# Optimization experiments

Measured on AMD Instinct MI355X. Metric: run time of the kernel, lower is better.

The kernel has to match this reference:

```python
import jax, jax.numpy as jnp
import numpy as np
import math

NUM_HEADS = 16
EMBED_DIM = 1024
DIM_HEAD = EMBED_DIM // NUM_HEADS


def setup_inputs() -> dict:
    key = jax.random.key(0)
    k_x, k_wi, k_bi, k_wo, k_bo = jax.random.split(key, 5)
    B, S, D = 2, 2048, EMBED_DIM
    scale = 1.0 / math.sqrt(D)
    return {
        "x": jax.random.normal(k_x, (B, S, D), dtype=jnp.float32),
        "w_in": jax.random.normal(k_wi, (3 * D, D), dtype=jnp.float32) * scale,
        "b_in": jax.random.normal(k_bi, (3 * D,), dtype=jnp.float32) * 0.02,
        "w_out": jax.random.normal(k_wo, (D, D), dtype=jnp.float32) * scale,
        "b_out": jax.random.normal(k_bo, (D,), dtype=jnp.float32) * 0.02,
    }


def reference(x, w_in, b_in, w_out, b_out):
    B, S, D = x.shape
    H, Dh = NUM_HEADS, DIM_HEAD
    # in_proj: x @ w_in.T + b_in -> chunk into q, k, v
    qkv = jnp.einsum("bsd,ed->bse", x, w_in) + b_in  # [B,S,3D]
    q, k, v = jnp.split(qkv, 3, axis=-1)
    q = q.reshape(B, S, H, Dh).transpose(0, 2, 1, 3)  # [B,H,S,Dh]
    k = k.reshape(B, S, H, Dh).transpose(0, 2, 1, 3)
    v = v.reshape(B, S, H, Dh).transpose(0, 2, 1, 3)
    # scores, causal mask (masked_fill before scaling == after, since -inf/c = -inf)
    scores = jnp.einsum("bhqd,bhkd->bhqk", q, k) / math.sqrt(Dh)
    causal = jnp.triu(jnp.ones((S, S), dtype=bool), k=1)
    scores = jnp.where(causal, -jnp.inf, scores)
    weight = jax.nn.softmax(scores, axis=-1)
    out = jnp.einsum("bhqk,bhkd->bhqd", weight, v)  # [B,H,S,Dh]
    out = out.transpose(0, 2, 1, 3).reshape(B, S, D)
    return jnp.einsum("bsd,ed->bse", out, w_out) + b_out
```

## Files before the change

kernel.cpp:

```cpp
#include <hip/hip_runtime.h>
#include <stdint.h>

typedef unsigned short u16;
typedef float f32x4 __attribute__((ext_vector_type(4)));
typedef __bf16 bf16x8 __attribute__((ext_vector_type(8)));

#define AS1 __attribute__((address_space(1)))
#define AS3 __attribute__((address_space(3)))

#define QK_SCALE 0.18033688011112042f

__device__ __forceinline__ u16 f32_to_bf16(float f) {
    unsigned u = __float_as_uint(f);
    unsigned r = u + 0x7fffu + ((u >> 16) & 1u);
    return (u16)(r >> 16);
}

__device__ __forceinline__ float bf16_f(u16 u) {
    return __uint_as_float(((unsigned)u) << 16);
}

__device__ __forceinline__ void gload_lds16(const u16* g, u16* l) {
    __builtin_amdgcn_global_load_lds((const AS1 unsigned int*)g,
                                     (AS3 unsigned int*)l, 16, 0, 0);
}

__device__ __forceinline__ int swz(int row, int col8) {
    return row * 64 + (((col8 ^ (row & 7)) & 7) << 3);
}
__device__ __forceinline__ int swzv(int row, int col8) {
    return row * 64 + (((col8 ^ row ^ (row >> 3)) & 7) << 3);
}

__global__ __launch_bounds__(256) void cvt_bf16_3(const float4* __restrict__ in0,
                                                  const float4* __restrict__ in1,
                                                  const float4* __restrict__ in2,
                                                  uint2* __restrict__ out,
                                                  int n0, int n1, int ntot) {
    for (int i = blockIdx.x * blockDim.x + threadIdx.x; i < ntot;
         i += gridDim.x * blockDim.x) {
        float4 v;
        if (i < n0) v = in0[i];
        else if (i < n0 + n1) {
            v = in1[i - n0];
            if (((i - n0) >> 8) < 1024) {
                v.x *= QK_SCALE; v.y *= QK_SCALE; v.z *= QK_SCALE; v.w *= QK_SCALE;
            }
        } else v = in2[i - n0 - n1];
        uint2 o;
        o.x = (unsigned)f32_to_bf16(v.x) | ((unsigned)f32_to_bf16(v.y) << 16);
        o.y = (unsigned)f32_to_bf16(v.z) | ((unsigned)f32_to_bf16(v.w) << 16);
        out[i] = o;
    }
}

template <int BNT, bool BF16_OUT>
__global__ __launch_bounds__(512, 2) void gemm_ring(const u16* __restrict__ A,
                                                    const u16* __restrict__ B,
                                                    const float* __restrict__ bias,
                                                    void* __restrict__ Cv,
                                                    int M, int N, int K,
                                                    int qcols, float qscale) {
    extern __shared__ u16 lds[];
    constexpr int NACC = BNT / 64;
    constexpr int NCH = (128 + BNT) >> 7;
    constexpr int ASZ = 128 * 32;
    constexpr int BSZ = BNT * 32;
    const int t = threadIdx.x;
    const int l = t & 63, w = t >> 6;
    const int lr = l & 15, lhi = l >> 4;
    const int wm = w >> 2, wn = w & 3;
    const int orig = blockIdx.y * gridDim.x + blockIdx.x;
    const int sid = (orig & 7) * 32 + (orig >> 3);
    const int bm = sid & 31, bn = sid >> 5;

    const u16* Ag = A + (size_t)bm * 128 * K;
    const u16* Bg = B + (size_t)bn * BNT * K;

    auto STAGE = [&](int kt, int slot) {
        u16* As = lds + slot * ASZ;
        u16* Bs = lds + 4 * ASZ + slot * BSZ;
        {
            int c = t, row = c >> 2, cp = c & 3;
            int gc = (cp ^ ((row >> 1) & 3)) << 3;
            gload_lds16(Ag + (size_t)row * K + kt * 32 + gc, As + c * 8);
        }
        #pragma unroll
        for (int i = 0; i < NCH - 1; ++i) {
            int c = i * 512 + t, row = c >> 2, cp = c & 3;
            int gc = (cp ^ ((row >> 1) & 3)) << 3;
            gload_lds16(Bg + (size_t)row * K + kt * 32 + gc, Bs + c * 8);
        }
    };

    f32x4 acc[4][NACC] = {};
    const int NT = K >> 5;
    STAGE(0, 0);
    STAGE(1, 1);
    STAGE(2, 2);

    const int ckey = (lr >> 1) & 3;

    for (int kt = 0; kt < NT; ++kt) {
        if (kt < NT - 2) {
            if constexpr (NCH == 4) asm volatile("s_waitcnt vmcnt(8)" ::: "memory");
            else                    asm volatile("s_waitcnt vmcnt(4)" ::: "memory");
        } else if (kt == NT - 2) {
            if constexpr (NCH == 4) asm volatile("s_waitcnt vmcnt(4)" ::: "memory");
            else                    asm volatile("s_waitcnt vmcnt(2)" ::: "memory");
        } else {
            asm volatile("s_waitcnt vmcnt(0)" ::: "memory");
        }
        __builtin_amdgcn_s_barrier();
        __builtin_amdgcn_sched_barrier(0);

        if (kt + 3 < NT) STAGE(kt + 3, (kt + 3) & 3);

        const u16* As = lds + (kt & 3) * ASZ;
        const u16* Bs = lds + 4 * ASZ + (kt & 3) * BSZ;
        bf16x8 af[4], bfv[NACC];
        #pragma unroll
        for (int m = 0; m < 4; ++m) {
            int row = wm * 64 + m * 16 + lr;
            af[m] = *(const bf16x8*)(As + row * 32 + ((lhi ^ ckey) << 3));
        }
        #pragma unroll
        for (int n = 0; n < NACC; ++n) {
            int row = wn * (BNT / 4) + n * 16 + lr;
            bfv[n] = *(const bf16x8*)(Bs + row * 32 + ((lhi ^ ckey) << 3));
        }
        __builtin_amdgcn_s_setprio(1);
        #pragma unroll
        for (int m = 0; m < 4; ++m)
            #pragma unroll
            for (int n = 0; n < NACC; ++n)
                acc[m][n] = __builtin_amdgcn_mfma_f32_16x16x32_bf16(
                    af[m], bfv[n], acc[m][n], 0, 0, 0);
        __builtin_amdgcn_s_setprio(0);
    }

    const int row0 = bm * 128 + wm * 64 + lhi * 4;
    const int col0 = bn * BNT + wn * (BNT / 4) + lr;
    #pragma unroll
    for (int n = 0; n < NACC; ++n) {
        int col = col0 + n * 16;
        float bv = bias[col];
        if (col < qcols) bv *= qscale;
        #pragma unroll
        for (int m = 0; m < 4; ++m)
            #pragma unroll
            for (int r = 0; r < 4; ++r) {
                int row = row0 + m * 16 + r;
                float v = acc[m][n][r] + bv;
                if constexpr (BF16_OUT)
                    ((u16*)Cv)[(size_t)row * N + col] = f32_to_bf16(v);
                else
                    ((float*)Cv)[(size_t)row * N + col] = v;
            }
    }
}

__device__ __forceinline__ void write_vt(u16* vt, uint4 a, uint4 b, int g, int cl) {
    unsigned aw[4] = {a.x, a.y, a.z, a.w};
    unsigned bw[4] = {b.x, b.y, b.z, b.w};
    #pragma unroll
    for (int j = 0; j < 8; ++j) {
        int dh = cl * 8 + j;
        unsigned sel = (j & 1) ? 0x07060302u : 0x05040100u;
        unsigned v = __builtin_amdgcn_perm(bw[j >> 1], aw[j >> 1], sel);
        *(unsigned*)(vt + swzv(dh, g >> 2) + (2 * g & 7)) = v;
    }
}

__global__ __launch_bounds__(512, 4) void attn_kernel(const u16* __restrict__ qkv,
                                                      u16* __restrict__ out) {
    __shared__ u16 Ks[2][2][64 * 64];
    __shared__ u16 Vt[2][64 * 64];
    __shared__ u16 Ps[8][16 * 64];
    const int t = threadIdx.x;
    const int w = t >> 6, l = t & 63;
    const int lr = l & 15, lhi = l >> 4;
    const int par = w >> 2, wl = w & 3;
    const int tp = t & 255;
    const int orig = blockIdx.x;
    const int sid = (orig & 7) * 64 + (orig >> 3);
    const int bh = sid >> 4, bi = sid & 15;
    const int h = bh & 15, b = bh >> 4;

    const u16* Kg = qkv + ((size_t)(b * 2048)) * 3072 + 1024 + h * 64;
    const u16* Vg = qkv + ((size_t)(b * 2048)) * 3072 + 2048 + h * 64;
    const int vg = tp >> 3, vcl = tp & 7;
    u16* Pw = Ps[w];
    unsigned* Pst = (unsigned*)Pw;
    float2* mlX = (float2*)&Ks[0][0][0];

    #pragma unroll 1
    for (int pass = 0; pass < 2; ++pass) {
        const int qt = pass ? (31 - bi) : bi;
        __syncthreads();

        const u16* Qrow = qkv + ((size_t)(b * 2048 + qt * 64 + wl * 16 + lr)) * 3072 + h * 64;
        bf16x8 qf0 = *(const bf16x8*)(Qrow + lhi * 8);
        bf16x8 qf1 = *(const bf16x8*)(Qrow + 32 + lhi * 8);

        uint4 va = {0, 0, 0, 0}, vbr = {0, 0, 0, 0};
        if (par <= qt) {
            #pragma unroll
            for (int i = 0; i < 2; ++i) {
                int c = i * 256 + tp, r = c >> 3, cl = c & 7;
                gload_lds16(Kg + ((size_t)(par * 64 + r)) * 3072 + ((cl ^ (r & 7)) << 3),
                            &Ks[par][0][c * 8]);
            }
            va = *(const uint4*)(Vg + ((size_t)(par * 64 + 2 * vg)) * 3072 + vcl * 8);
            vbr = *(const uint4*)(Vg + ((size_t)(par * 64 + 2 * vg + 1)) * 3072 + vcl * 8);
            write_vt(Vt[par], va, vbr, vg, vcl);
        }
        __syncthreads();

        f32x4 acc[4] = {};
        float m_run = -1e30f, l_run = 0.f;
        int cur = 0;
        const int nt = (qt >> 1) + 1;

        for (int it = 0; it < nt; ++it) {
            const int t64 = 2 * it + par;
            const bool active = (t64 <= qt);
            const bool pfv = (t64 + 2 <= qt);
            if (pfv) {
                #pragma unroll
                for (int i = 0; i < 2; ++i) {
                    int c = i * 256 + tp, r = c >> 3, cl = c & 7;
                    gload_lds16(Kg + ((size_t)((t64 + 2) * 64 + r)) * 3072 +
                                    ((cl ^ (r & 7)) << 3),
                                &Ks[par][cur ^ 1][c * 8]);
                }
                va = *(const uint4*)(Vg + ((size_t)((t64 + 2) * 64 + 2 * vg)) * 3072 + vcl * 8);
                vbr = *(const uint4*)(Vg + ((size_t)((t64 + 2) * 64 + 2 * vg + 1)) * 3072 + vcl * 8);
            }

            if (active) {
                f32x4 sv[4] = {};
                __builtin_amdgcn_s_setprio(1);
                #pragma unroll
                for (int kks = 0; kks < 2; ++kks) {
                    #pragma unroll
                    for (int n = 0; n < 4; ++n) {
                        bf16x8 kf = *(const bf16x8*)(&Ks[par][cur][swz(n * 16 + lr, kks * 4 + lhi)]);
                        sv[n] = __builtin_amdgcn_mfma_f32_16x16x32_bf16(
                            kf, kks ? qf1 : qf0, sv[n], 0, 0, 0);
                    }
                }
                __builtin_amdgcn_s_setprio(0);

                if (t64 == qt) {
                    #pragma unroll
                    for (int n = 0; n < 4; ++n)
                        #pragma unroll
                        for (int r = 0; r < 4; ++r)
                            if ((n * 16 + lhi * 4 + r) > (wl * 16 + lr)) sv[n][r] = -1e30f;
                }
                float t0 = fmaxf(fmaxf(sv[0][0], sv[0][1]), fmaxf(sv[0][2], sv[0][3]));
                float t1 = fmaxf(fmaxf(sv[1][0], sv[1][1]), fmaxf(sv[1][2], sv[1][3]));
                float t2 = fmaxf(fmaxf(sv[2][0], sv[2][1]), fmaxf(sv[2][2], sv[2][3]));
                float t3 = fmaxf(fmaxf(sv[3][0], sv[3][1]), fmaxf(sv[3][2], sv[3][3]));
                float mx = fmaxf(fmaxf(t0, t1), fmaxf(t2, t3));
                mx = fmaxf(mx, __shfl_xor(mx, 16, 64));
                mx = fmaxf(mx, __shfl_xor(mx, 32, 64));

                if (__any(mx > m_run + 8.f)) {
                    float mn = fmaxf(m_run, mx);
                    float alpha = exp2f(m_run - mn);
                    m_run = mn;
                    l_run *= alpha;
                    #pragma unroll
                    for (int r = 0; r < 4; ++r) {
                        float ar = __shfl(alpha, lhi * 4 + r, 16);
                        #pragma unroll
                        for (int n = 0; n < 4; ++n) acc[n][r] *= ar;
                    }
                }

                float rs = 0.f;
                #pragma unroll
                for (int n = 0; n < 4; ++n)
                    #pragma unroll
                    for (int r = 0; r < 4; ++r) {
                        float pe = exp2f(sv[n][r] - m_run);
                        sv[n][r] = pe;
                        rs += pe;
                    }
                l_run += rs;

                #pragma unroll
                for (int n = 0; n < 4; ++n)
                    #pragma unroll
                    for (int rp = 0; rp < 2; ++rp) {
                        union { unsigned u; __bf16 hh[2]; } pk;
                        pk.hh[0] = (__bf16)sv[n][2 * rp];
                        pk.hh[1] = (__bf16)sv[n][2 * rp + 1];
                        int pp = 8 * n + 2 * lhi + rp;
                        Pst[lr * 32 + (((pp >> 2) ^ (lr & 7)) << 2) + (pp & 3)] = pk.u;
                    }

                __builtin_amdgcn_s_setprio(1);
                #pragma unroll
                for (int kks = 0; kks < 2; ++kks) {
                    bf16x8 pa = *(const bf16x8*)(Pw + lr * 64 +
                                                 (((kks * 4 + lhi) ^ (lr & 7)) << 3));
                    #pragma unroll
                    for (int n = 0; n < 4; ++n) {
                        bf16x8 vb = *(const bf16x8*)(&Vt[par][swzv(n * 16 + lr, kks * 4 + lhi)]);
                        acc[n] = __builtin_amdgcn_mfma_f32_16x16x32_bf16(pa, vb, acc[n], 0, 0, 0);
                    }
                }
                __builtin_amdgcn_s_setprio(0);
            }

            __syncthreads();
            if (pfv) write_vt(Vt[par], va, vbr, vg, vcl);
            __syncthreads();
            cur ^= 1;
        }

        l_run += __shfl_xor(l_run, 16, 64);
        l_run += __shfl_xor(l_run, 32, 64);

        if (par == 1) {
            if (lhi == 0) mlX[wl * 16 + lr] = make_float2(m_run, l_run);
            #pragma unroll
            for (int r = 0; r < 4; ++r)
                #pragma unroll
                for (int n = 0; n < 4; ++n)
                    Pw[(lhi * 4 + r) * 64 + n * 16 + lr] = f32_to_bf16(acc[n][r]);
        }
        __syncthreads();
        if (par == 0) {
            float2 m1l1 = mlX[wl * 16 + lr];
            float m = fmaxf(m_run, m1l1.x);
            float e0 = exp2f(m_run - m), e1 = exp2f(m1l1.x - m);
            float inv = 1.0f / (l_run * e0 + m1l1.y * e1);
            float c0 = e0 * inv, c1 = e1 * inv;
            const u16* Pq = Ps[4 + wl];
            #pragma unroll
            for (int r = 0; r < 4; ++r) {
                float c0r = __shfl(c0, lhi * 4 + r, 16);
                float c1r = __shfl(c1, lhi * 4 + r, 16);
                int qg = qt * 64 + wl * 16 + lhi * 4 + r;
                size_t base = ((size_t)(b * 2048 + qg)) * 1024 + h * 64;
                #pragma unroll
                for (int n = 0; n < 4; ++n) {
                    float v1 = bf16_f(Pq[(lhi * 4 + r) * 64 + n * 16 + lr]);
                    out[base + n * 16 + lr] = f32_to_bf16(acc[n][r] * c0r + v1 * c1r);
                }
            }
        }
    }
}

extern "C" void kernel_launch(void* const* d_in, const int* in_sizes, int n_in,
                              void* d_out, int out_size, void* d_ws, size_t ws_size,
                              hipStream_t stream) {
    const float* x = (const float*)d_in[0];
    const float* w_in = (const float*)d_in[1];
    const float* b_in = (const float*)d_in[2];
    const float* w_out = (const float*)d_in[3];
    const float* b_out = (const float*)d_in[4];
    float* out = (float*)d_out;

    u16* xb = (u16*)d_ws;
    u16* wib = xb + (size_t)4096 * 1024;
    u16* wob = wib + (size_t)3072 * 1024;
    u16* qkvb = wob + (size_t)1024 * 1024;
    u16* attnb = qkvb + (size_t)4096 * 3072;

    const int n0 = 4096 * 1024 / 4, n1 = 3072 * 1024 / 4, n2 = 1024 * 1024 / 4;
    cvt_bf16_3<<<2048, 256, 0, stream>>>((const float4*)x, (const float4*)w_in,
                                         (const float4*)w_out, (uint2*)xb,
                                         n0, n1, n0 + n1 + n2);

    (void)hipFuncSetAttribute((const void*)gemm_ring<384, true>,
                              hipFuncAttributeMaxDynamicSharedMemorySize, 131072);
    (void)hipFuncSetAttribute((const void*)gemm_ring<128, false>,
                              hipFuncAttributeMaxDynamicSharedMemorySize, 65536);

    gemm_ring<384, true><<<dim3(32, 8), 512, 131072, stream>>>(
        xb, wib, b_in, qkvb, 4096, 3072, 1024, 1024, QK_SCALE);
    attn_kernel<<<512, 512, 0, stream>>>(qkvb, attnb);
    gemm_ring<128, false><<<dim3(32, 8), 512, 65536, stream>>>(
        attnb, wob, b_out, out, 4096, 1024, 1024, 0, 1.0f);
}
```

Measured before the change: 105.4 us.

## Split paired attention passes into one block per query tile with register-staged K

Each attention block previously processed two query tiles (bi and 31-bi) in sequence for load balance. Now each block handles a single query tile, heaviest first, with 1024 blocks launched. The K double buffer in LDS is replaced by prefetching K into registers and writing it after the barrier, the same way V already was. The launch bound rises to 6 blocks per CU to raise occupancy. P stores become 64-bit. The trade-off is more blocks with uneven work, more register pressure, and losing the async global-to-LDS K loads.

Result: slower. 185.8 us (+76.3%).

```diff
diff --git a/kernel.cpp b/kernel.cpp
--- a/kernel.cpp
+++ b/kernel.cpp
@@ -172,9 +172,9 @@
     }
 }
 
-__global__ __launch_bounds__(512, 4) void attn_kernel(const u16* __restrict__ qkv,
+__global__ __launch_bounds__(512, 6) void attn_kernel(const u16* __restrict__ qkv,
                                                       u16* __restrict__ out) {
-    __shared__ u16 Ks[2][2][64 * 64];
+    __shared__ u16 Ks[2][64 * 64];
     __shared__ u16 Vt[2][64 * 64];
     __shared__ u16 Ps[8][16 * 64];
     const int t = threadIdx.x;
@@ -183,175 +183,167 @@
     const int par = w >> 2, wl = w & 3;
     const int tp = t & 255;
     const int orig = blockIdx.x;
-    const int sid = (orig & 7) * 64 + (orig >> 3);
-    const int bh = sid >> 4, bi = sid & 15;
+    const int sid = (orig & 7) * 128 + (orig >> 3);
+    const int bh = sid >> 5;
+    const int qt = 31 - (sid & 31);
     const int h = bh & 15, b = bh >> 4;
 
     const u16* Kg = qkv + ((size_t)(b * 2048)) * 3072 + 1024 + h * 64;
     const u16* Vg = qkv + ((size_t)(b * 2048)) * 3072 + 2048 + h * 64;
     const int vg = tp >> 3, vcl = tp & 7;
+    const int kr0 = tp >> 3, kc0 = ((tp & 7) ^ (kr0 & 7)) << 3;
+    const int kr1 = (256 + tp) >> 3, kc1 = ((tp & 7) ^ (kr1 & 7)) << 3;
     u16* Pw = Ps[w];
     unsigned* Pst = (unsigned*)Pw;
-    float2* mlX = (float2*)&Ks[0][0][0];
-
-    #pragma unroll 1
-    for (int pass = 0; pass < 2; ++pass) {
-        const int qt = pass ? (31 - bi) : bi;
-        __syncthreads();
-
-        const u16* Qrow = qkv + ((size_t)(b * 2048 + qt * 64 + wl * 16 + lr)) * 3072 + h * 64;
-        bf16x8 qf0 = *(const bf16x8*)(Qrow + lhi * 8);
-        bf16x8 qf1 = *(const bf16x8*)(Qrow + 32 + lhi * 8);
-
-        uint4 va = {0, 0, 0, 0}, vbr = {0, 0, 0, 0};
-        if (par <= qt) {
-            #pragma unroll
-            for (int i = 0; i < 2; ++i) {
-                int c = i * 256 + tp, r = c >> 3, cl = c & 7;
-                gload_lds16(Kg + ((size_t)(par * 64 + r)) * 3072 + ((cl ^ (r & 7)) << 3),
-                            &Ks[par][0][c * 8]);
-            }
-            va = *(const uint4*)(Vg + ((size_t)(par * 64 + 2 * vg)) * 3072 + vcl * 8);
-            vbr = *(const uint4*)(Vg + ((size_t)(par * 64 + 2 * vg + 1)) * 3072 + vcl * 8);
-            write_vt(Vt[par], va, vbr, vg, vcl);
-        }
-        __syncthreads();
-
-        f32x4 acc[4] = {};
-        float m_run = -1e30f, l_run = 0.f;
-        int cur = 0;
-        const int nt = (qt >> 1) + 1;
-
-        for (int it = 0; it < nt; ++it) {
-            const int t64 = 2 * it + par;
-            const bool active = (t64 <= qt);
-            const bool pfv = (t64 + 2 <= qt);
-            if (pfv) {
-                #pragma unroll
-                for (int i = 0; i < 2; ++i) {
-                    int c = i * 256 + tp, r = c >> 3, cl = c & 7;
-                    gload_lds16(Kg + ((size_t)((t64 + 2) * 64 + r)) * 3072 +
-                                    ((cl ^ (r & 7)) << 3),
-                                &Ks[par][cur ^ 1][c * 8]);
+    float2* mlX = (float2*)&Ks[0][0];
+
+    const u16* Qrow = qkv + ((size_t)(b * 2048 + qt * 64 + wl * 16 + lr)) * 3072 + h * 64;
+    bf16x8 qf0 = *(const bf16x8*)(Qrow + lhi * 8);
+    bf16x8 qf1 = *(const bf16x8*)(Qrow + 32 + lhi * 8);
+
+    if (par <= qt) {
+        uint4 ka = *(const uint4*)(Kg + ((size_t)(par * 64 + kr0)) * 3072 + kc0);
+        uint4 kb = *(const uint4*)(Kg + ((size_t)(par * 64 + kr1)) * 3072 + kc1);
+        uint4 va = *(const uint4*)(Vg + ((size_t)(par * 64 + 2 * vg)) * 3072 + vcl * 8);
+        uint4 vbr = *(const uint4*)(Vg + ((size_t)(par * 64 + 2 * vg + 1)) * 3072 + vcl * 8);
+        ((uint4*)Ks[par])[tp] = ka;
+        ((uint4*)Ks[par])[256 + tp] = kb;
+        write_vt(Vt[par], va, vbr, vg, vcl);
+    }
+    __syncthreads();
+
+    f32x4 acc[4] = {};
+    float m_run = -1e30f, l_run = 0.f;
+    const int nt = (qt >> 1) + 1;
+
+    for (int it = 0; it < nt; ++it) {
+        const int t64 = 2 * it + par;
+        const bool active = (t64 <= qt);
+        const bool pfv = (t64 + 2 <= qt);
+        uint4 ka, kb, va, vbr;
+        if (pfv) {
+            ka = *(const uint4*)(Kg + ((size_t)((t64 + 2) * 64 + kr0)) * 3072 + kc0);
+            kb = *(const uint4*)(Kg + ((size_t)((t64 + 2) * 64 + kr1)) * 3072 + kc1);
+            va = *(const uint4*)(Vg + ((size_t)((t64 + 2) * 64 + 2 * vg)) * 3072 + vcl * 8);
+            vbr = *(const uint4*)(Vg + ((size_t)((t64 + 2) * 64 + 2 * vg + 1)) * 3072 + vcl * 8);
+        }
+
+        if (active) {
+            f32x4 sv[4] = {};
+            __builtin_amdgcn_s_setprio(1);
+            #pragma unroll
+            for (int kks = 0; kks < 2; ++kks) {
+                #pragma unroll
+                for (int n = 0; n < 4; ++n) {
+                    bf16x8 kf = *(const bf16x8*)(&Ks[par][swz(n * 16 + lr, kks * 4 + lhi)]);
+                    sv[n] = __builtin_amdgcn_mfma_f32_16x16x32_bf16(
+                        kf, kks ? qf1 : qf0, sv[n], 0, 0, 0);
                 }
-                va = *(const uint4*)(Vg + ((size_t)((t64 + 2) * 64 + 2 * vg)) * 3072 + vcl * 8);
-                vbr = *(const uint4*)(Vg + ((size_t)((t64 + 2) * 64 + 2 * vg + 1)) * 3072 + vcl * 8);
-            }
-
-            if (active) {
-                f32x4 sv[4] = {};
-                __builtin_amdgcn_s_setprio(1);
-                #pragma unroll
-                for (int kks = 0; kks < 2; ++kks) {
-                    #pragma unroll
-                    for (int n = 0; n < 4; ++n) {
-                        bf16x8 kf = *(const bf16x8*)(&Ks[par][cur][swz(n * 16 + lr, kks * 4 + lhi)]);
-                        sv[n] = __builtin_amdgcn_mfma_f32_16x16x32_bf16(
-                            kf, kks ? qf1 : qf0, sv[n], 0, 0, 0);
-                    }
-                }
-                __builtin_amdgcn_s_setprio(0);
-
-                if (t64 == qt) {
-                    #pragma unroll
-                    for (int n = 0; n < 4; ++n)
-                        #pragma unroll
-                        for (int r = 0; r < 4; ++r)
-                            if ((n * 16 + lhi * 4 + r) > (wl * 16 + lr)) sv[n][r] = -1e30f;
-                }
-                float t0 = fmaxf(fmaxf(sv[0][0], sv[0][1]), fmaxf(sv[0][2], sv[0][3]));
-                float t1 = fmaxf(fmaxf(sv[1][0], sv[1][1]), fmaxf(sv[1][2], sv[1][3]));
-                float t2 = fmaxf(fmaxf(sv[2][0], sv[2][1]), fmaxf(sv[2][2], sv[2][3]));
-                float t3 = fmaxf(fmaxf(sv[3][0], sv[3][1]), fmaxf(sv[3][2], sv[3][3]));
-                float mx = fmaxf(fmaxf(t0, t1), fmaxf(t2, t3));
-                mx = fmaxf(mx, __shfl_xor(mx, 16, 64));
-                mx = fmaxf(mx, __shfl_xor(mx, 32, 64));
-
-                if (__any(mx > m_run + 8.f)) {
-                    float mn = fmaxf(m_run, mx);
-                    float alpha = exp2f(m_run - mn);
-                    m_run = mn;
-                    l_run *= alpha;
-                    #pragma unroll
-                    for (int r = 0; r < 4; ++r) {
-                        float ar = __shfl(alpha, lhi * 4 + r, 16);
-                        #pragma unroll
-                        for (int n = 0; n < 4; ++n) acc[n][r] *= ar;
-                    }
-                }
-
-                float rs = 0.f;
+            }
+            __builtin_amdgcn_s_setprio(0);
+
+            if (t64 == qt) {
                 #pragma unroll
                 for (int n = 0; n < 4; ++n)
                     #pragma unroll
-                    for (int r = 0; r < 4; ++r) {
-                        float pe = exp2f(sv[n][r] - m_run);
-                        sv[n][r] = pe;
-                        rs += pe;
-                    }
-                l_run += rs;
-
-                #pragma unroll
-                for (int n = 0; n < 4; ++n)
+                    for (int r = 0; r < 4; ++r)
+                        if ((n * 16 + lhi * 4 + r) > (wl * 16 + lr)) sv[n][r] = -1e30f;
+            }
+            float t0 = fmaxf(fmaxf(sv[0][0], sv[0][1]), fmaxf(sv[0][2], sv[0][3]));
+            float t1 = fmaxf(fmaxf(sv[1][0], sv[1][1]), fmaxf(sv[1][2], sv[1][3]));
+            float t2 = fmaxf(fmaxf(sv[2][0], sv[2][1]), fmaxf(sv[2][2], sv[2][3]));
+            float t3 = fmaxf(fmaxf(sv[3][0], sv[3][1]), fmaxf(sv[3][2], sv[3][3]));
+            float mx = fmaxf(fmaxf(t0, t1), fmaxf(t2, t3));
+            mx = fmaxf(mx, __shfl_xor(mx, 16, 64));
+            mx = fmaxf(mx, __shfl_xor(mx, 32, 64));
+
+            if (__any(mx > m_run + 8.f)) {
+                float mn = fmaxf(m_run, mx);
+                float alpha = exp2f(m_run - mn);
+                m_run = mn;
+                l_run *= alpha;
+                #pragma unroll
+                for (int r = 0; r < 4; ++r) {
+                    float ar = __shfl(alpha, lhi * 4 + r, 16);
                     #pragma unroll
-                    for (int rp = 0; rp < 2; ++rp) {
-                        union { unsigned u; __bf16 hh[2]; } pk;
-                        pk.hh[0] = (__bf16)sv[n][2 * rp];
-                        pk.hh[1] = (__bf16)sv[n][2 * rp + 1];
-                        int pp = 8 * n + 2 * lhi + rp;
-                        Pst[lr * 32 + (((pp >> 2) ^ (lr & 7)) << 2) + (pp & 3)] = pk.u;
-                    }
-
-                __builtin_amdgcn_s_setprio(1);
-                #pragma unroll
-                for (int kks = 0; kks < 2; ++kks) {
-                    bf16x8 pa = *(const bf16x8*)(Pw + lr * 64 +
-                                                 (((kks * 4 + lhi) ^ (lr & 7)) << 3));
-                    #pragma unroll
-                    for (int n = 0; n < 4; ++n) {
-                        bf16x8 vb = *(const bf16x8*)(&Vt[par][swzv(n * 16 + lr, kks * 4 + lhi)]);
-                        acc[n] = __builtin_amdgcn_mfma_f32_16x16x32_bf16(pa, vb, acc[n], 0, 0, 0);
-                    }
+                    for (int n = 0; n < 4; ++n) acc[n][r] *= ar;
                 }
-                __builtin_amdgcn_s_setprio(0);
-            }
-
-            __syncthreads();
-            if (pfv) write_vt(Vt[par], va, vbr, vg, vcl);
-            __syncthreads();
-            cur ^= 1;
-        }
-
-        l_run += __shfl_xor(l_run, 16, 64);
-        l_run += __shfl_xor(l_run, 32, 64);
-
-        if (par == 1) {
-            if (lhi == 0) mlX[wl * 16 + lr] = make_float2(m_run, l_run);
-            #pragma unroll
-            for (int r = 0; r < 4; ++r)
-                #pragma unroll
-                for (int n = 0; n < 4; ++n)
-                    Pw[(lhi * 4 + r) * 64 + n * 16 + lr] = f32_to_bf16(acc[n][r]);
-        }
+            }
+
+            float rs = 0.f;
+            #pragma unroll
+            for (int n = 0; n < 4; ++n)
+                #pragma unroll
+                for (int r = 0; r < 4; ++r) {
+                    float pe = exp2f(sv[n][r] - m_run);
+                    sv[n][r] = pe;
+                    rs += pe;
+                }
+            l_run += rs;
+
+            #pragma unroll
+            for (int n = 0; n < 4; ++n) {
+                union { uint2 u2; __bf16 hh[4]; } pk;
+                pk.hh[0] = (__bf16)sv[n][0];
+                pk.hh[1] = (__bf16)sv[n][1];
+                pk.hh[2] = (__bf16)sv[n][2];
+                pk.hh[3] = (__bf16)sv[n][3];
+                int pp = 8 * n + 2 * lhi;
+                *(uint2*)&Pst[lr * 32 + (((pp >> 2) ^ (lr & 7)) << 2) + (pp & 3)] = pk.u2;
+            }
+
+            __builtin_amdgcn_s_setprio(1);
+            #pragma unroll
+            for (int kks = 0; kks < 2; ++kks) {
+                bf16x8 pa = *(const bf16x8*)(Pw + lr * 64 +
+                                             (((kks * 4 + lhi) ^ (lr & 7)) << 3));
+                #pragma unroll
+                for (int n = 0; n < 4; ++n) {
+                    bf16x8 vb = *(const bf16x8*)(&Vt[par][swzv(n * 16 + lr, kks * 4 + lhi)]);
+                    acc[n] = __builtin_amdgcn_mfma_f32_16x16x32_bf16(pa, vb, acc[n], 0, 0, 0);
+                }
+            }
+            __builtin_amdgcn_s_setprio(0);
+        }
+
         __syncthreads();
-        if (par == 0) {
-            float2 m1l1 = mlX[wl * 16 + lr];
-            float m = fmaxf(m_run, m1l1.x);
-            float e0 = exp2f(m_run - m), e1 = exp2f(m1l1.x - m);
-            float inv = 1.0f / (l_run * e0 + m1l1.y * e1);
-            float c0 = e0 * inv, c1 = e1 * inv;
-            const u16* Pq = Ps[4 + wl];
-            #pragma unroll
-            for (int r = 0; r < 4; ++r) {
-                float c0r = __shfl(c0, lhi * 4 + r, 16);
-                float c1r = __shfl(c1, lhi * 4 + r, 16);
-                int qg = qt * 64 + wl * 16 + lhi * 4 + r;
-                size_t base = ((size_t)(b * 2048 + qg)) * 1024 + h * 64;
-                #pragma unroll
-                for (int n = 0; n < 4; ++n) {
-                    float v1 = bf16_f(Pq[(lhi * 4 + r) * 64 + n * 16 + lr]);
-                    out[base + n * 16 + lr] = f32_to_bf16(acc[n][r] * c0r + v1 * c1r);
-                }
+        if (pfv) {
+            ((uint4*)Ks[par])[tp] = ka;
+            ((uint4*)Ks[par])[256 + tp] = kb;
+            write_vt(Vt[par], va, vbr, vg, vcl);
+        }
+        __syncthreads();
+    }
+
+    l_run += __shfl_xor(l_run, 16, 64);
+    l_run += __shfl_xor(l_run, 32, 64);
+
+    if (par == 1) {
+        if (lhi == 0) mlX[wl * 16 + lr] = make_float2(m_run, l_run);
+        #pragma unroll
+        for (int r = 0; r < 4; ++r)
+            #pragma unroll
+            for (int n = 0; n < 4; ++n)
+                Pw[(lhi * 4 + r) * 64 + n * 16 + lr] = f32_to_bf16(acc[n][r]);
+    }
+    __syncthreads();
+    if (par == 0) {
+        float2 m1l1 = mlX[wl * 16 + lr];
+        float m = fmaxf(m_run, m1l1.x);
+        float e0 = exp2f(m_run - m), e1 = exp2f(m1l1.x - m);
+        float inv = 1.0f / (l_run * e0 + m1l1.y * e1);
+        float c0 = e0 * inv, c1 = e1 * inv;
+        const u16* Pq = Ps[4 + wl];
+        #pragma unroll
+        for (int r = 0; r < 4; ++r) {
+            float c0r = __shfl(c0, lhi * 4 + r, 16);
+            float c1r = __shfl(c1, lhi * 4 + r, 16);
+            int qg = qt * 64 + wl * 16 + lhi * 4 + r;
+            size_t base = ((size_t)(b * 2048 + qg)) * 1024 + h * 64;
+            #pragma unroll
+            for (int n = 0; n < 4; ++n) {
+                float v1 = bf16_f(Pq[(lhi * 4 + r) * 64 + n * 16 + lr]);
+                out[base + n * 16 + lr] = f32_to_bf16(acc[n][r] * c0r + v1 * c1r);
             }
         }
     }
@@ -385,7 +377,7 @@
 
     gemm_ring<384, true><<<dim3(32, 8), 512, 131072, stream>>>(
         xb, wib, b_in, qkvb, 4096, 3072, 1024, 1024, QK_SCALE);
-    attn_kernel<<<512, 512, 0, stream>>>(qkvb, attnb);
+    attn_kernel<<<1024, 512, 0, stream>>>(qkvb, attnb);
     gemm_ring<128, false><<<dim3(32, 8), 512, 65536, stream>>>(
         attnb, wob, b_out, out, 4096, 1024, 1024, 0, 1.0f);
 }
```
